# Kernel tuning notes

Measured on AMD Instinct MI355X. Metric: run time of the kernel, lower is better.

Reference implementation:

```python
import jax, jax.numpy as jnp
import numpy as np

NUM_EXPERTS = 8
TOP_K = 2
B, L, H = 4, 4096, 1024


def setup_inputs() -> dict:
    key = jax.random.key(0)
    ks = jax.random.split(key, 5)
    s = 1.0 / np.sqrt(H)
    return {
        "hidden_states": jax.random.normal(ks[0], (B, L, H), dtype=jnp.float32),
        "gate_w": jax.random.normal(ks[1], (H, NUM_EXPERTS), dtype=jnp.float32) * s,
        "w1": jax.random.normal(ks[2], (NUM_EXPERTS, H, 2 * H), dtype=jnp.float32) * s,
        "b1": jnp.zeros((NUM_EXPERTS, 2 * H), dtype=jnp.float32),
        "w2": jax.random.normal(ks[3], (NUM_EXPERTS, 2 * H, H), dtype=jnp.float32) * (1.0 / np.sqrt(2 * H)),
        "b2": jnp.zeros((NUM_EXPERTS, H), dtype=jnp.float32),
    }


def reference(hidden_states, gate_w, w1, b1, w2, b2):
    b, l, h = hidden_states.shape
    flat = hidden_states.reshape(-1, h)                      # [T, H]
    router_logits = flat @ gate_w                            # [T, E]
    probs = jax.nn.softmax(router_logits, axis=-1)
    weights, indices = jax.lax.top_k(probs, TOP_K)           # [T, K]
    weights = weights / jnp.sum(weights, axis=-1, keepdims=True)
    # combine[t, e] = sum_k weights[t, k] * 1{indices[t, k] == e}
    onehot = jax.nn.one_hot(indices, NUM_EXPERTS, dtype=flat.dtype)  # [T, K, E]
    combine = jnp.einsum('tk,tke->te', weights, onehot)      # [T, E]
    out = jnp.zeros_like(flat)
    for e in range(NUM_EXPERTS):  # fixed small expert loop; dense-compute, sparse-combine
        hdn = jax.nn.relu(flat @ w1[e] + b1[e])              # [T, 2H]
        y = hdn @ w2[e] + b2[e]                              # [T, H]
        out = out + combine[:, e:e + 1] * y
    return out.reshape(b, l, h)
```

## Files before the change

### kernel.cpp

```cpp
#include <hip/hip_runtime.h>
#include <hip/hip_bf16.h>
#include <stdint.h>

#define T_TOK 16384
#define HD    1024
#define HD2   2048
#define NE    8
#define ROWS  (2*T_TOK)
#define MAXT  264
#define MT256 136
#define RTOK  32

#define M_NT    256
#define M_OFFS  272
#define M_TILES 288

typedef __bf16 bf16x8 __attribute__((ext_vector_type(8)));
typedef float f32x4 __attribute__((ext_vector_type(4)));

#define GLD16(g, l) __builtin_amdgcn_global_load_lds( \
    (const __attribute__((address_space(1))) void*)(g), \
    (__attribute__((address_space(3))) void*)(l), 16, 0, 0)

__device__ inline unsigned short f2bf(float f) {
    unsigned int u = __float_as_uint(f);
    unsigned int r = (u + 0x7fffu + ((u >> 16) & 1u)) >> 16;
    return (unsigned short)r;
}

__global__ __launch_bounds__(256) void cvt_wT(const float* __restrict__ w,
                                              unsigned short* __restrict__ wt,
                                              int K, int N) {
    __shared__ float t[32][33];
    int e = blockIdx.z;
    int n0 = blockIdx.x * 32, k0 = blockIdx.y * 32;
    int r = threadIdx.x >> 3;
    int c4 = (threadIdx.x & 7) * 4;
    const float* src = w + ((size_t)e * K + k0 + r) * N + n0 + c4;
    float4 v = *(const float4*)src;
    t[r][c4] = v.x; t[r][c4+1] = v.y; t[r][c4+2] = v.z; t[r][c4+3] = v.w;
    __syncthreads();
    int cc = threadIdx.x & 7;
    ushort4 o;
    o.x = f2bf(t[cc*4+0][r]); o.y = f2bf(t[cc*4+1][r]);
    o.z = f2bf(t[cc*4+2][r]); o.w = f2bf(t[cc*4+3][r]);
    *(ushort4*)(wt + ((size_t)e * N + n0 + r) * K + k0 + cc*4) = o;
}

__global__ __launch_bounds__(256) void router_k(const float* __restrict__ x,
        const float* __restrict__ gw, int* __restrict__ meta,
        int* __restrict__ tok_e, int* __restrict__ tok_slot, float* __restrict__ tok_w,
        unsigned short* __restrict__ xb) {
    __shared__ float g[NE * HD];
    __shared__ int   le[RTOK * 2];
    __shared__ float lw[RTOK * 2];
    __shared__ int   lslot[RTOK * 2];
    __shared__ int   lcnt[NE];
    __shared__ int   lbase[NE];
    for (int i = threadIdx.x; i < NE * HD; i += 256) {
        int k = i >> 3, e = i & 7;
        g[e * HD + k] = gw[i];
    }
    if (threadIdx.x < NE) lcnt[threadIdx.x] = 0;
    __syncthreads();

    int wave = threadIdx.x >> 6, lane = threadIdx.x & 63;
    int t0 = blockIdx.x * RTOK;
    for (int i = 0; i < RTOK / 4; i++) {
        int tt = wave * (RTOK / 4) + i;
        int t = t0 + tt;
        const float4* xr = (const float4*)(x + (size_t)t * HD);
        float acc[NE];
#pragma unroll
        for (int e = 0; e < NE; e++) acc[e] = 0.f;
#pragma unroll
        for (int j = 0; j < HD / 256; j++) {
            float4 xv = xr[lane + 64 * j];
            ushort4 o4;
            o4.x = f2bf(xv.x); o4.y = f2bf(xv.y);
            o4.z = f2bf(xv.z); o4.w = f2bf(xv.w);
            *(ushort4*)(xb + (size_t)t * HD + (lane + 64 * j) * 4) = o4;
#pragma unroll
            for (int e = 0; e < NE; e++) {
                float4 gv = *(const float4*)&g[e * HD + (lane + 64 * j) * 4];
                acc[e] += xv.x * gv.x + xv.y * gv.y + xv.z * gv.z + xv.w * gv.w;
            }
        }
#pragma unroll
        for (int e = 0; e < NE; e++) {
            float v = acc[e];
#pragma unroll
            for (int off = 32; off > 0; off >>= 1) v += __shfl_down(v, off, 64);
            acc[e] = v;
        }
        if (lane == 0) {
            int e1 = 0; float l1 = acc[0];
#pragma unroll
            for (int e = 1; e < NE; e++) if (acc[e] > l1) { l1 = acc[e]; e1 = e; }
            int e2 = -1; float l2 = -3.0e38f;
#pragma unroll
            for (int e = 0; e < NE; e++) if (e != e1 && acc[e] > l2) { l2 = acc[e]; e2 = e; }
            float w1 = 1.f / (1.f + expf(l2 - l1));
            le[tt * 2] = e1;     le[tt * 2 + 1] = e2;
            lw[tt * 2] = w1;     lw[tt * 2 + 1] = 1.f - w1;
        }
    }
    __syncthreads();
    if (threadIdx.x < RTOK * 2)
        lslot[threadIdx.x] = atomicAdd(&lcnt[le[threadIdx.x]], 1);
    __syncthreads();
    if (threadIdx.x < NE)
        lbase[threadIdx.x] = atomicAdd(&meta[threadIdx.x * 32], lcnt[threadIdx.x]);
    __syncthreads();
    if (threadIdx.x < RTOK * 2) {
        int gi = t0 * 2 + threadIdx.x;
        int e = le[threadIdx.x];
        tok_e[gi]    = e;
        tok_slot[gi] = lbase[e] + lslot[threadIdx.x];
        tok_w[gi]    = lw[threadIdx.x];
    }
}

__global__ __launch_bounds__(64) void offsets_k(int* __restrict__ meta) {
    int lane = threadIdx.x;
    int cl = (lane < NE) ? meta[lane * 32] : 0;
    int cnt[NE], offs[NE], tbase[NE];
    int o = 0, tb = 0;
#pragma unroll
    for (int e = 0; e < NE; e++) {
        cnt[e] = __shfl(cl, e, 64);
        offs[e] = o;  o += cnt[e];
        tbase[e] = tb; tb += (cnt[e] + 255) >> 8;
    }
    int nt = tb;
    if (lane == 0) meta[M_NT] = nt;
    if (lane < NE) meta[M_OFFS + lane] = offs[lane];
    for (int i = lane; i < nt; i += 64) {
        int e = 0;
#pragma unroll
        for (int k = 1; k < NE; k++) if (i >= tbase[k]) e = k;
        int m = i - tbase[e];
        int r0 = offs[e] + m * 256;
        int re = offs[e] + cnt[e];
        if (r0 + 256 < re) re = r0 + 256;
        meta[M_TILES + i] = e;
        meta[M_TILES + MAXT + i] = r0;
        meta[M_TILES + 2 * MAXT + i] = re;
    }
}

__global__ __launch_bounds__(256) void scatter_k(const int* __restrict__ meta,
        const int* __restrict__ tok_e, const int* __restrict__ tok_slot,
        const float* __restrict__ tok_w, int* __restrict__ rows_tok,
        float* __restrict__ rows_w) {
    int i = blockIdx.x * 256 + threadIdx.x;
    const int* offs = meta + M_OFFS;
    int e = tok_e[i];
    int r = offs[e] + tok_slot[i];
    rows_tok[r] = i >> 1;
    rows_w[r] = tok_w[i];
}


#define ISSUE(KK, NT_) do { \
    int kk_ = (KK) < (NT_) ? (KK) : (NT_) - 1; \
    int bb_ = ((KK) & 3) * 8192; \
    GLD16(pa0 + kk_ * 32, &As[bb_ + (w * 64) * 8]); \
    GLD16(pa1 + kk_ * 32, &As[bb_ + (512 + w * 64) * 8]); \
    GLD16(pb0 + kk_ * 32, &Bs[bb_ + (w * 64) * 8]); \
    GLD16(pb1 + kk_ * 32, &Bs[bb_ + (512 + w * 64) * 8]); } while (0)
#define SB0()   __builtin_amdgcn_sched_barrier(0)
#define VMW12() do { asm volatile("s_waitcnt vmcnt(12)" ::: "memory"); SB0(); } while (0)
#define VMW0()  do { asm volatile("s_waitcnt vmcnt(0)" ::: "memory"); SB0(); } while (0)
#define BAR()   do { __builtin_amdgcn_s_barrier(); SB0(); } while (0)

#define KSTEP(RB) do { \
    bf16x8 af[4], bfr[2][2]; \
    _Pragma("unroll") \
    for (int bh_ = 0; bh_ < 2; bh_++) \
    _Pragma("unroll") \
    for (int in_ = 0; in_ < 2; in_++) { \
        int row_ = bh_ * 128 + wn * 32 + in_ * 16 + rl; \
        int ph_ = q ^ ((row_ >> 1) & 3); \
        bfr[bh_][in_] = *(const bf16x8*)&Bs[(RB) + row_ * 32 + ph_ * 8]; \
    } \
    _Pragma("unroll") \
    for (int ah_ = 0; ah_ < 2; ah_++) { \
        _Pragma("unroll") \
        for (int im_ = 0; im_ < 4; im_++) { \
            int row_ = ah_ * 128 + wm * 64 + im_ * 16 + rl; \
            int ph_ = q ^ ((row_ >> 1) & 3); \
            af[im_] = *(const bf16x8*)&As[(RB) + row_ * 32 + ph_ * 8]; \
        } \
        _Pragma("unroll") \
        for (int im_ = 0; im_ < 4; im_++) \
        _Pragma("unroll") \
        for (int bh_ = 0; bh_ < 2; bh_++) \
        _Pragma("unroll") \
        for (int in_ = 0; in_ < 2; in_++) \
            acc[ah_][bh_][im_][in_] = __builtin_amdgcn_mfma_f32_16x16x32_bf16( \
                af[im_], bfr[bh_][in_], acc[ah_][bh_][im_][in_], 0, 0, 0); \
    } } while (0)

__global__ __launch_bounds__(512, 2) void gemm1_k(
    const unsigned short* __restrict__ Xbf,
    const unsigned short* __restrict__ W1T,
    const float* __restrict__ b1,
    const int* __restrict__ meta,
    const int* __restrict__ rows_tok,
    unsigned short* __restrict__ hdn)
{
    __shared__ unsigned short As[4 * 8192];
    __shared__ unsigned short Bs[4 * 8192];
    int nt = meta[M_NT];
    int fid = blockIdx.y * 8 + blockIdx.x;
    int lid = (fid & 7) * MT256 + (fid >> 3);
    int xx = lid & 7, mt = lid >> 3;
    if (mt >= nt) return;
    int e    = meta[M_TILES + mt];
    int r0   = meta[M_TILES + MAXT + mt];
    int rend = meta[M_TILES + 2 * MAXT + mt];
    int n0 = xx * 256;

    int tid = threadIdx.x, w = tid >> 6, lane = tid & 63;
    int wm = w >> 2, wn = w & 3;
    int rl = lane & 15, q = lane >> 4;

    const unsigned short *pa0, *pa1, *pb0, *pb1;
    {
        int gg = tid, row = gg >> 2, lc = (gg & 3) ^ ((row >> 1) & 3);
        int grow = r0 + row; grow = grow < ROWS - 1 ? grow : ROWS - 1;
        pa0 = Xbf + (size_t)rows_tok[grow] * HD + lc * 8;
        pb0 = W1T + ((size_t)e * HD2 + n0 + row) * HD + lc * 8;
        gg = 512 + tid; row = gg >> 2; lc = (gg & 3) ^ ((row >> 1) & 3);
        grow = r0 + row; grow = grow < ROWS - 1 ? grow : ROWS - 1;
        pa1 = Xbf + (size_t)rows_tok[grow] * HD + lc * 8;
        pb1 = W1T + ((size_t)e * HD2 + n0 + row) * HD + lc * 8;
    }

    f32x4 acc[2][2][4][2];
#pragma unroll
    for (int a = 0; a < 2; a++)
#pragma unroll
    for (int b = 0; b < 2; b++)
#pragma unroll
    for (int i = 0; i < 4; i++)
#pragma unroll
    for (int n = 0; n < 2; n++)
        acc[a][b][i][n] = (f32x4){0.f, 0.f, 0.f, 0.f};

    ISSUE(0, HD / 32); ISSUE(1, HD / 32); ISSUE(2, HD / 32);

#pragma unroll 4
    for (int kt = 0; kt < HD / 32; kt++) {
        ISSUE(kt + 3, HD / 32);
        SB0();
        VMW12();
        BAR();
        KSTEP((kt & 3) * 8192);
        BAR();
    }
    VMW0();

    const float* b1e = b1 + (size_t)e * HD2;
#pragma unroll
    for (int ah = 0; ah < 2; ah++)
#pragma unroll
    for (int bh = 0; bh < 2; bh++)
#pragma unroll
    for (int in = 0; in < 2; in++) {
        int col = n0 + bh * 128 + wn * 32 + in * 16 + rl;
        float bias = b1e[col];
#pragma unroll
        for (int im = 0; im < 4; im++) {
            int rb2 = r0 + ah * 128 + wm * 64 + im * 16 + q * 4;
#pragma unroll
            for (int j = 0; j < 4; j++) {
                int r = rb2 + j;
                if (r < rend) {
                    float v = acc[ah][bh][im][in][j] + bias;
                    v = v > 0.f ? v : 0.f;
                    hdn[(size_t)r * HD2 + col] = f2bf(v);
                }
            }
        }
    }
}

__global__ __launch_bounds__(512, 2) void gemm2_k(
    const unsigned short* __restrict__ hdn,
    const unsigned short* __restrict__ W2T,
    const float* __restrict__ b2,
    const int* __restrict__ meta,
    const int* __restrict__ rows_tok,
    const float* __restrict__ rows_w,
    float* __restrict__ out)
{
    __shared__ unsigned short As[4 * 8192];
    __shared__ unsigned short Bs[4 * 8192];
    int nt = meta[M_NT];
    int fid = blockIdx.y * 4 + blockIdx.x;
    int lid = (fid & 7) * (MT256 / 2) + (fid >> 3);
    int xx = lid & 3, mt = lid >> 2;
    if (mt >= nt) return;
    int e    = meta[M_TILES + mt];
    int r0   = meta[M_TILES + MAXT + mt];
    int rend = meta[M_TILES + 2 * MAXT + mt];
    int n0 = xx * 256;

    int tid = threadIdx.x, w = tid >> 6, lane = tid & 63;
    int wm = w >> 2, wn = w & 3;
    int rl = lane & 15, q = lane >> 4;

    const unsigned short *pa0, *pa1, *pb0, *pb1;
    {
        int gg = tid, row = gg >> 2, lc = (gg & 3) ^ ((row >> 1) & 3);
        int grow = r0 + row; grow = grow < ROWS - 1 ? grow : ROWS - 1;
        pa0 = hdn + (size_t)grow * HD2 + lc * 8;
        pb0 = W2T + ((size_t)e * HD + n0 + row) * HD2 + lc * 8;
        gg = 512 + tid; row = gg >> 2; lc = (gg & 3) ^ ((row >> 1) & 3);
        grow = r0 + row; grow = grow < ROWS - 1 ? grow : ROWS - 1;
        pa1 = hdn + (size_t)grow * HD2 + lc * 8;
        pb1 = W2T + ((size_t)e * HD + n0 + row) * HD2 + lc * 8;
    }

    f32x4 acc[2][2][4][2];
#pragma unroll
    for (int a = 0; a < 2; a++)
#pragma unroll
    for (int b = 0; b < 2; b++)
#pragma unroll
    for (int i = 0; i < 4; i++)
#pragma unroll
    for (int n = 0; n < 2; n++)
        acc[a][b][i][n] = (f32x4){0.f, 0.f, 0.f, 0.f};

    ISSUE(0, HD2 / 32); ISSUE(1, HD2 / 32); ISSUE(2, HD2 / 32);

#pragma unroll 4
    for (int kt = 0; kt < HD2 / 32; kt++) {
        ISSUE(kt + 3, HD2 / 32);
        SB0();
        VMW12();
        BAR();
        KSTEP((kt & 3) * 8192);
        BAR();
    }
    VMW0();

    const float* b2e = b2 + (size_t)e * HD;
    float bias[2][2];
#pragma unroll
    for (int bh = 0; bh < 2; bh++)
#pragma unroll
        for (int in = 0; in < 2; in++)
            bias[bh][in] = b2e[n0 + bh * 128 + wn * 32 + in * 16 + rl];
#pragma unroll
    for (int ah = 0; ah < 2; ah++)
#pragma unroll
    for (int im = 0; im < 4; im++) {
        int rb2 = r0 + ah * 128 + wm * 64 + im * 16 + q * 4;
#pragma unroll
        for (int j = 0; j < 4; j++) {
            int r = rb2 + j;
            if (r < rend) {
                int tok = rows_tok[r];
                float wt = rows_w[r];
                float* op = out + (size_t)tok * HD + n0;
#pragma unroll
                for (int bh = 0; bh < 2; bh++)
#pragma unroll
                for (int in = 0; in < 2; in++) {
                    float v = (acc[ah][bh][im][in][j] + bias[bh][in]) * wt;
                    atomicAdd(op + bh * 128 + wn * 32 + in * 16 + rl, v);
                }
            }
        }
    }
}

extern "C" void kernel_launch(void* const* d_in, const int* in_sizes, int n_in,
                              void* d_out, int out_size, void* d_ws, size_t ws_size,
                              hipStream_t stream) {
    const float* x  = (const float*)d_in[0];
    const float* gw = (const float*)d_in[1];
    const float* w1 = (const float*)d_in[2];
    const float* b1 = (const float*)d_in[3];
    const float* w2 = (const float*)d_in[4];
    const float* b2 = (const float*)d_in[5];
    float* out = (float*)d_out;

    uint8_t* ws = (uint8_t*)d_ws;
    unsigned short* Xbf = (unsigned short*)(ws);
    unsigned short* W1T = (unsigned short*)(ws + 33554432ull);
    unsigned short* W2T = (unsigned short*)(ws + 67108864ull);
    unsigned short* HDN = (unsigned short*)(ws + 100663296ull);
    int*   meta     = (int*)(ws + 234881024ull);
    int*   tok_e    = meta + 2048;
    int*   tok_slot = tok_e + ROWS;
    float* tok_w    = (float*)(tok_slot + ROWS);
    int*   rows_tok = (int*)(tok_w + ROWS);
    float* rows_w   = (float*)(rows_tok + ROWS);

    hipMemsetAsync(meta, 0, 1024, stream);
    hipMemsetAsync(d_out, 0, (size_t)out_size * sizeof(float), stream);

    cvt_wT<<<dim3(HD2 / 32, HD / 32, NE), 256, 0, stream>>>(w1, W1T, HD, HD2);
    cvt_wT<<<dim3(HD / 32, HD2 / 32, NE), 256, 0, stream>>>(w2, W2T, HD2, HD);
    router_k<<<T_TOK / RTOK, 256, 0, stream>>>(x, gw, meta, tok_e, tok_slot, tok_w, Xbf);
    offsets_k<<<1, 64, 0, stream>>>(meta);
    scatter_k<<<ROWS / 256, 256, 0, stream>>>(meta, tok_e, tok_slot, tok_w, rows_tok, rows_w);
    gemm1_k<<<dim3(HD2 / 256, MT256), 512, 0, stream>>>(Xbf, W1T, b1, meta, rows_tok, HDN);
    gemm2_k<<<dim3(HD / 256, MT256), 512, 0, stream>>>(HDN, W2T, b2, meta, rows_tok, rows_w, out);
}
```

Measured before the change: 756.5 us.

## Process two K-steps per barrier, raise MFMA priority, balance tiles across XCD groups

Both expert GEMM kernels now consume two 32-wide K slices between each barrier pair. They issue the next two slices together and wait with vmcnt(8) instead of vmcnt(12). This halves the number of workgroup barriers per tile, at the cost of a shorter effective prefetch distance for the second slice in each pair. The MFMA section is wrapped in s_setprio(1)/s_setprio(0) so waves doing math get issue priority. The block-to-tile mapping is also changed to split only the live tiles evenly across the 8 block groups (likely one per XCD), instead of a fixed MT256 stride that left some groups idle.

```diff
diff --git a/kernel.cpp b/kernel.cpp
--- a/kernel.cpp
+++ b/kernel.cpp
@@ -170,9 +170,10 @@
     GLD16(pb0 + kk_ * 32, &Bs[bb_ + (w * 64) * 8]); \
     GLD16(pb1 + kk_ * 32, &Bs[bb_ + (512 + w * 64) * 8]); } while (0)
 #define SB0()   __builtin_amdgcn_sched_barrier(0)
-#define VMW12() do { asm volatile("s_waitcnt vmcnt(12)" ::: "memory"); SB0(); } while (0)
+#define VMW8()  do { asm volatile("s_waitcnt vmcnt(8)" ::: "memory"); SB0(); } while (0)
 #define VMW0()  do { asm volatile("s_waitcnt vmcnt(0)" ::: "memory"); SB0(); } while (0)
 #define BAR()   do { __builtin_amdgcn_s_barrier(); SB0(); } while (0)
+#define PRIO(P) __builtin_amdgcn_s_setprio(P)
 
 #define KSTEP(RB) do { \
     bf16x8 af[4], bfr[2][2]; \
@@ -214,9 +215,13 @@
     __shared__ unsigned short Bs[4 * 8192];
     int nt = meta[M_NT];
     int fid = blockIdx.y * 8 + blockIdx.x;
-    int lid = (fid & 7) * MT256 + (fid >> 3);
+    int nwork = nt * 8;
+    int x = fid & 7, i = fid >> 3;
+    int qq = nwork >> 3, rr = nwork & 7;
+    int mine = qq + (x < rr ? 1 : 0);
+    if (i >= mine) return;
+    int lid = x * qq + (x < rr ? x : rr) + i;
     int xx = lid & 7, mt = lid >> 3;
-    if (mt >= nt) return;
     int e    = meta[M_TILES + mt];
     int r0   = meta[M_TILES + MAXT + mt];
     int rend = meta[M_TILES + 2 * MAXT + mt];
@@ -244,20 +249,24 @@
 #pragma unroll
     for (int b = 0; b < 2; b++)
 #pragma unroll
-    for (int i = 0; i < 4; i++)
+    for (int i2 = 0; i2 < 4; i2++)
 #pragma unroll
     for (int n = 0; n < 2; n++)
-        acc[a][b][i][n] = (f32x4){0.f, 0.f, 0.f, 0.f};
-
-    ISSUE(0, HD / 32); ISSUE(1, HD / 32); ISSUE(2, HD / 32);
-
-#pragma unroll 4
-    for (int kt = 0; kt < HD / 32; kt++) {
-        ISSUE(kt + 3, HD / 32);
+        acc[a][b][i2][n] = (f32x4){0.f, 0.f, 0.f, 0.f};
+
+    ISSUE(0, HD / 32); ISSUE(1, HD / 32);
+
+#pragma unroll 2
+    for (int bt = 0; bt < HD / 64; bt++) {
+        int t = 2 * bt;
+        ISSUE(t + 2, HD / 32); ISSUE(t + 3, HD / 32);
         SB0();
-        VMW12();
+        VMW8();
         BAR();
-        KSTEP((kt & 3) * 8192);
+        PRIO(1);
+        KSTEP((t & 3) * 8192);
+        KSTEP(((t + 1) & 3) * 8192);
+        PRIO(0);
         BAR();
     }
     VMW0();
@@ -300,9 +309,13 @@
     __shared__ unsigned short Bs[4 * 8192];
     int nt = meta[M_NT];
     int fid = blockIdx.y * 4 + blockIdx.x;
-    int lid = (fid & 7) * (MT256 / 2) + (fid >> 3);
+    int nwork = nt * 4;
+    int x = fid & 7, i = fid >> 3;
+    int qq = nwork >> 3, rr = nwork & 7;
+    int mine = qq + (x < rr ? 1 : 0);
+    if (i >= mine) return;
+    int lid = x * qq + (x < rr ? x : rr) + i;
     int xx = lid & 3, mt = lid >> 2;
-    if (mt >= nt) return;
     int e    = meta[M_TILES + mt];
     int r0   = meta[M_TILES + MAXT + mt];
     int rend = meta[M_TILES + 2 * MAXT + mt];
@@ -330,20 +343,24 @@
 #pragma unroll
     for (int b = 0; b < 2; b++)
 #pragma unroll
-    for (int i = 0; i < 4; i++)
+    for (int i2 = 0; i2 < 4; i2++)
 #pragma unroll
     for (int n = 0; n < 2; n++)
-        acc[a][b][i][n] = (f32x4){0.f, 0.f, 0.f, 0.f};
-
-    ISSUE(0, HD2 / 32); ISSUE(1, HD2 / 32); ISSUE(2, HD2 / 32);
-
-#pragma unroll 4
-    for (int kt = 0; kt < HD2 / 32; kt++) {
-        ISSUE(kt + 3, HD2 / 32);
+        acc[a][b][i2][n] = (f32x4){0.f, 0.f, 0.f, 0.f};
+
+    ISSUE(0, HD2 / 32); ISSUE(1, HD2 / 32);
+
+#pragma unroll 2
+    for (int bt = 0; bt < HD2 / 64; bt++) {
+        int t = 2 * bt;
+        ISSUE(t + 2, HD2 / 32); ISSUE(t + 3, HD2 / 32);
         SB0();
-        VMW12();
+        VMW8();
         BAR();
-        KSTEP((kt & 3) * 8192);
+        PRIO(1);
+        KSTEP((t & 3) * 8192);
+        KSTEP(((t + 1) & 3) * 8192);
+        PRIO(0);
         BAR();
     }
     VMW0();
```

Result: slower. 791.4 us (+4.6%).

## Shrink MoE GEMM tiles to 128x128 with 256-thread blocks and double buffering

Applied to the files above, without the earlier changes.

Both expert GEMMs move from 256x256 tiles with 512 threads and a 4-stage LDS pipeline to 128x128 tiles with 256 threads, double-buffered LDS, and 4 blocks per CU. The routing offsets kernel now builds 128-row tiles, and the grouped tile-to-block swizzle is dropped in favour of direct blockIdx mapping. MFMA sections are wrapped in s_setprio. The aim is less padding waste on per-expert tails and more concurrent blocks, at the cost of lower arithmetic intensity per tile, a shallower prefetch pipeline and more redundant weight loads.

```diff
diff --git a/kernel.cpp b/kernel.cpp
--- a/kernel.cpp
+++ b/kernel.cpp
@@ -8,7 +8,6 @@
 #define NE    8
 #define ROWS  (2*T_TOK)
 #define MAXT  264
-#define MT256 136
 #define RTOK  32
 
 #define M_NT    256
@@ -130,7 +129,7 @@
     for (int e = 0; e < NE; e++) {
         cnt[e] = __shfl(cl, e, 64);
         offs[e] = o;  o += cnt[e];
-        tbase[e] = tb; tb += (cnt[e] + 255) >> 8;
+        tbase[e] = tb; tb += (cnt[e] + 127) >> 7;
     }
     int nt = tb;
     if (lane == 0) meta[M_NT] = nt;
@@ -140,9 +139,9 @@
 #pragma unroll
         for (int k = 1; k < NE; k++) if (i >= tbase[k]) e = k;
         int m = i - tbase[e];
-        int r0 = offs[e] + m * 256;
+        int r0 = offs[e] + m * 128;
         int re = offs[e] + cnt[e];
-        if (r0 + 256 < re) re = r0 + 256;
+        if (r0 + 128 < re) re = r0 + 128;
         meta[M_TILES + i] = e;
         meta[M_TILES + MAXT + i] = r0;
         meta[M_TILES + 2 * MAXT + i] = re;
@@ -164,45 +163,39 @@
 
 #define ISSUE(KK, NT_) do { \
     int kk_ = (KK) < (NT_) ? (KK) : (NT_) - 1; \
-    int bb_ = ((KK) & 3) * 8192; \
+    int bb_ = ((KK) & 1) * 4096; \
     GLD16(pa0 + kk_ * 32, &As[bb_ + (w * 64) * 8]); \
-    GLD16(pa1 + kk_ * 32, &As[bb_ + (512 + w * 64) * 8]); \
+    GLD16(pa1 + kk_ * 32, &As[bb_ + (256 + w * 64) * 8]); \
     GLD16(pb0 + kk_ * 32, &Bs[bb_ + (w * 64) * 8]); \
-    GLD16(pb1 + kk_ * 32, &Bs[bb_ + (512 + w * 64) * 8]); } while (0)
+    GLD16(pb1 + kk_ * 32, &Bs[bb_ + (256 + w * 64) * 8]); } while (0)
 #define SB0()   __builtin_amdgcn_sched_barrier(0)
-#define VMW12() do { asm volatile("s_waitcnt vmcnt(12)" ::: "memory"); SB0(); } while (0)
+#define VMW4()  do { asm volatile("s_waitcnt vmcnt(4)" ::: "memory"); SB0(); } while (0)
 #define VMW0()  do { asm volatile("s_waitcnt vmcnt(0)" ::: "memory"); SB0(); } while (0)
 #define BAR()   do { __builtin_amdgcn_s_barrier(); SB0(); } while (0)
+#define PRIO(P) __builtin_amdgcn_s_setprio(P)
 
 #define KSTEP(RB) do { \
-    bf16x8 af[4], bfr[2][2]; \
+    bf16x8 af[4], bfr[4]; \
     _Pragma("unroll") \
-    for (int bh_ = 0; bh_ < 2; bh_++) \
-    _Pragma("unroll") \
-    for (int in_ = 0; in_ < 2; in_++) { \
-        int row_ = bh_ * 128 + wn * 32 + in_ * 16 + rl; \
+    for (int in_ = 0; in_ < 4; in_++) { \
+        int row_ = wn * 64 + in_ * 16 + rl; \
         int ph_ = q ^ ((row_ >> 1) & 3); \
-        bfr[bh_][in_] = *(const bf16x8*)&Bs[(RB) + row_ * 32 + ph_ * 8]; \
+        bfr[in_] = *(const bf16x8*)&Bs[(RB) + row_ * 32 + ph_ * 8]; \
     } \
     _Pragma("unroll") \
-    for (int ah_ = 0; ah_ < 2; ah_++) { \
-        _Pragma("unroll") \
-        for (int im_ = 0; im_ < 4; im_++) { \
-            int row_ = ah_ * 128 + wm * 64 + im_ * 16 + rl; \
-            int ph_ = q ^ ((row_ >> 1) & 3); \
-            af[im_] = *(const bf16x8*)&As[(RB) + row_ * 32 + ph_ * 8]; \
-        } \
-        _Pragma("unroll") \
-        for (int im_ = 0; im_ < 4; im_++) \
-        _Pragma("unroll") \
-        for (int bh_ = 0; bh_ < 2; bh_++) \
-        _Pragma("unroll") \
-        for (int in_ = 0; in_ < 2; in_++) \
-            acc[ah_][bh_][im_][in_] = __builtin_amdgcn_mfma_f32_16x16x32_bf16( \
-                af[im_], bfr[bh_][in_], acc[ah_][bh_][im_][in_], 0, 0, 0); \
-    } } while (0)
-
-__global__ __launch_bounds__(512, 2) void gemm1_k(
+    for (int im_ = 0; im_ < 4; im_++) { \
+        int row_ = wm * 64 + im_ * 16 + rl; \
+        int ph_ = q ^ ((row_ >> 1) & 3); \
+        af[im_] = *(const bf16x8*)&As[(RB) + row_ * 32 + ph_ * 8]; \
+    } \
+    _Pragma("unroll") \
+    for (int im_ = 0; im_ < 4; im_++) \
+    _Pragma("unroll") \
+    for (int in_ = 0; in_ < 4; in_++) \
+        acc[im_][in_] = __builtin_amdgcn_mfma_f32_16x16x32_bf16( \
+            af[im_], bfr[in_], acc[im_][in_], 0, 0, 0); } while (0)
+
+__global__ __launch_bounds__(256, 4) void gemm1_k(
     const unsigned short* __restrict__ Xbf,
     const unsigned short* __restrict__ W1T,
     const float* __restrict__ b1,
@@ -210,20 +203,18 @@
     const int* __restrict__ rows_tok,
     unsigned short* __restrict__ hdn)
 {
-    __shared__ unsigned short As[4 * 8192];
-    __shared__ unsigned short Bs[4 * 8192];
+    __shared__ unsigned short As[2 * 4096];
+    __shared__ unsigned short Bs[2 * 4096];
     int nt = meta[M_NT];
-    int fid = blockIdx.y * 8 + blockIdx.x;
-    int lid = (fid & 7) * MT256 + (fid >> 3);
-    int xx = lid & 7, mt = lid >> 3;
+    int mt = blockIdx.y;
     if (mt >= nt) return;
     int e    = meta[M_TILES + mt];
     int r0   = meta[M_TILES + MAXT + mt];
     int rend = meta[M_TILES + 2 * MAXT + mt];
-    int n0 = xx * 256;
+    int n0 = blockIdx.x * 128;
 
     int tid = threadIdx.x, w = tid >> 6, lane = tid & 63;
-    int wm = w >> 2, wn = w & 3;
+    int wm = w & 1, wn = w >> 1;
     int rl = lane & 15, q = lane >> 4;
 
     const unsigned short *pa0, *pa1, *pb0, *pb1;
@@ -232,53 +223,47 @@
         int grow = r0 + row; grow = grow < ROWS - 1 ? grow : ROWS - 1;
         pa0 = Xbf + (size_t)rows_tok[grow] * HD + lc * 8;
         pb0 = W1T + ((size_t)e * HD2 + n0 + row) * HD + lc * 8;
-        gg = 512 + tid; row = gg >> 2; lc = (gg & 3) ^ ((row >> 1) & 3);
+        gg = 256 + tid; row = gg >> 2; lc = (gg & 3) ^ ((row >> 1) & 3);
         grow = r0 + row; grow = grow < ROWS - 1 ? grow : ROWS - 1;
         pa1 = Xbf + (size_t)rows_tok[grow] * HD + lc * 8;
         pb1 = W1T + ((size_t)e * HD2 + n0 + row) * HD + lc * 8;
     }
 
-    f32x4 acc[2][2][4][2];
-#pragma unroll
-    for (int a = 0; a < 2; a++)
-#pragma unroll
-    for (int b = 0; b < 2; b++)
-#pragma unroll
-    for (int i = 0; i < 4; i++)
-#pragma unroll
-    for (int n = 0; n < 2; n++)
-        acc[a][b][i][n] = (f32x4){0.f, 0.f, 0.f, 0.f};
-
-    ISSUE(0, HD / 32); ISSUE(1, HD / 32); ISSUE(2, HD / 32);
-
-#pragma unroll 4
+    f32x4 acc[4][4];
+#pragma unroll
+    for (int a = 0; a < 4; a++)
+#pragma unroll
+    for (int b = 0; b < 4; b++)
+        acc[a][b] = (f32x4){0.f, 0.f, 0.f, 0.f};
+
+    ISSUE(0, HD / 32);
+
+#pragma unroll 2
     for (int kt = 0; kt < HD / 32; kt++) {
-        ISSUE(kt + 3, HD / 32);
+        ISSUE(kt + 1, HD / 32);
         SB0();
-        VMW12();
+        VMW4();
         BAR();
-        KSTEP((kt & 3) * 8192);
+        PRIO(1);
+        KSTEP((kt & 1) * 4096);
+        PRIO(0);
         BAR();
     }
     VMW0();
 
     const float* b1e = b1 + (size_t)e * HD2;
 #pragma unroll
-    for (int ah = 0; ah < 2; ah++)
-#pragma unroll
-    for (int bh = 0; bh < 2; bh++)
-#pragma unroll
-    for (int in = 0; in < 2; in++) {
-        int col = n0 + bh * 128 + wn * 32 + in * 16 + rl;
+    for (int in = 0; in < 4; in++) {
+        int col = n0 + wn * 64 + in * 16 + rl;
         float bias = b1e[col];
 #pragma unroll
         for (int im = 0; im < 4; im++) {
-            int rb2 = r0 + ah * 128 + wm * 64 + im * 16 + q * 4;
+            int rb2 = r0 + wm * 64 + im * 16 + q * 4;
 #pragma unroll
             for (int j = 0; j < 4; j++) {
                 int r = rb2 + j;
                 if (r < rend) {
-                    float v = acc[ah][bh][im][in][j] + bias;
+                    float v = acc[im][in][j] + bias;
                     v = v > 0.f ? v : 0.f;
                     hdn[(size_t)r * HD2 + col] = f2bf(v);
                 }
@@ -287,7 +272,7 @@
     }
 }
 
-__global__ __launch_bounds__(512, 2) void gemm2_k(
+__global__ __launch_bounds__(256, 4) void gemm2_k(
     const unsigned short* __restrict__ hdn,
     const unsigned short* __restrict__ W2T,
     const float* __restrict__ b2,
@@ -296,20 +281,18 @@
     const float* __restrict__ rows_w,
     float* __restrict__ out)
 {
-    __shared__ unsigned short As[4 * 8192];
-    __shared__ unsigned short Bs[4 * 8192];
+    __shared__ unsigned short As[2 * 4096];
+    __shared__ unsigned short Bs[2 * 4096];
     int nt = meta[M_NT];
-    int fid = blockIdx.y * 4 + blockIdx.x;
-    int lid = (fid & 7) * (MT256 / 2) + (fid >> 3);
-    int xx = lid & 3, mt = lid >> 2;
+    int mt = blockIdx.y;
     if (mt >= nt) return;
     int e    = meta[M_TILES + mt];
     int r0   = meta[M_TILES + MAXT + mt];
     int rend = meta[M_TILES + 2 * MAXT + mt];
-    int n0 = xx * 256;
+    int n0 = blockIdx.x * 128;
 
     int tid = threadIdx.x, w = tid >> 6, lane = tid & 63;
-    int wm = w >> 2, wn = w & 3;
+    int wm = w & 1, wn = w >> 1;
     int rl = lane & 15, q = lane >> 4;
 
     const unsigned short *pa0, *pa1, *pb0, *pb1;
@@ -318,61 +301,53 @@
         int grow = r0 + row; grow = grow < ROWS - 1 ? grow : ROWS - 1;
         pa0 = hdn + (size_t)grow * HD2 + lc * 8;
         pb0 = W2T + ((size_t)e * HD + n0 + row) * HD2 + lc * 8;
-        gg = 512 + tid; row = gg >> 2; lc = (gg & 3) ^ ((row >> 1) & 3);
+        gg = 256 + tid; row = gg >> 2; lc = (gg & 3) ^ ((row >> 1) & 3);
         grow = r0 + row; grow = grow < ROWS - 1 ? grow : ROWS - 1;
         pa1 = hdn + (size_t)grow * HD2 + lc * 8;
         pb1 = W2T + ((size_t)e * HD + n0 + row) * HD2 + lc * 8;
     }
 
-    f32x4 acc[2][2][4][2];
-#pragma unroll
-    for (int a = 0; a < 2; a++)
-#pragma unroll
-    for (int b = 0; b < 2; b++)
-#pragma unroll
-    for (int i = 0; i < 4; i++)
-#pragma unroll
-    for (int n = 0; n < 2; n++)
-        acc[a][b][i][n] = (f32x4){0.f, 0.f, 0.f, 0.f};
-
-    ISSUE(0, HD2 / 32); ISSUE(1, HD2 / 32); ISSUE(2, HD2 / 32);
-
-#pragma unroll 4
+    f32x4 acc[4][4];
+#pragma unroll
+    for (int a = 0; a < 4; a++)
+#pragma unroll
+    for (int b = 0; b < 4; b++)
+        acc[a][b] = (f32x4){0.f, 0.f, 0.f, 0.f};
+
+    ISSUE(0, HD2 / 32);
+
+#pragma unroll 2
     for (int kt = 0; kt < HD2 / 32; kt++) {
-        ISSUE(kt + 3, HD2 / 32);
+        ISSUE(kt + 1, HD2 / 32);
         SB0();
-        VMW12();
+        VMW4();
         BAR();
-        KSTEP((kt & 3) * 8192);
+        PRIO(1);
+        KSTEP((kt & 1) * 4096);
+        PRIO(0);
         BAR();
     }
     VMW0();
 
     const float* b2e = b2 + (size_t)e * HD;
-    float bias[2][2];
-#pragma unroll
-    for (int bh = 0; bh < 2; bh++)
-#pragma unroll
-        for (int in = 0; in < 2; in++)
-            bias[bh][in] = b2e[n0 + bh * 128 + wn * 32 + in * 16 + rl];
-#pragma unroll
-    for (int ah = 0; ah < 2; ah++)
+    float bias[4];
+#pragma unroll
+    for (int in = 0; in < 4; in++)
+        bias[in] = b2e[n0 + wn * 64 + in * 16 + rl];
 #pragma unroll
     for (int im = 0; im < 4; im++) {
-        int rb2 = r0 + ah * 128 + wm * 64 + im * 16 + q * 4;
+        int rb2 = r0 + wm * 64 + im * 16 + q * 4;
 #pragma unroll
         for (int j = 0; j < 4; j++) {
             int r = rb2 + j;
             if (r < rend) {
                 int tok = rows_tok[r];
                 float wt = rows_w[r];
-                float* op = out + (size_t)tok * HD + n0;
-#pragma unroll
-                for (int bh = 0; bh < 2; bh++)
-#pragma unroll
-                for (int in = 0; in < 2; in++) {
-                    float v = (acc[ah][bh][im][in][j] + bias[bh][in]) * wt;
-                    atomicAdd(op + bh * 128 + wn * 32 + in * 16 + rl, v);
+                float* op = out + (size_t)tok * HD + n0 + wn * 64;
+#pragma unroll
+                for (int in = 0; in < 4; in++) {
+                    float v = (acc[im][in][j] + bias[in]) * wt;
+                    atomicAdd(op + in * 16 + rl, v);
                 }
             }
         }
@@ -410,6 +385,6 @@
     router_k<<<T_TOK / RTOK, 256, 0, stream>>>(x, gw, meta, tok_e, tok_slot, tok_w, Xbf);
     offsets_k<<<1, 64, 0, stream>>>(meta);
     scatter_k<<<ROWS / 256, 256, 0, stream>>>(meta, tok_e, tok_slot, tok_w, rows_tok, rows_w);
-    gemm1_k<<<dim3(HD2 / 256, MT256), 512, 0, stream>>>(Xbf, W1T, b1, meta, rows_tok, HDN);
-    gemm2_k<<<dim3(HD / 256, MT256), 512, 0, stream>>>(HDN, W2T, b2, meta, rows_tok, rows_w, out);
-}
+    gemm1_k<<<dim3(HD2 / 128, MAXT), 256, 0, stream>>>(Xbf, W1T, b1, meta, rows_tok, HDN);
+    gemm2_k<<<dim3(HD / 128, MAXT), 256, 0, stream>>>(HDN, W2T, b2, meta, rows_tok, rows_w, out);
+}
```

Measured after the change: 730.8 us. -3.4%, faster.
